# Performance work log

Measured on AMD Instinct MI355X. Metric: run time of the kernel, lower is better.

Reference implementation:

```python
import jax, jax.numpy as jnp
import numpy as np

N_NODES = 50000
N_EDGES = 600000
N_ELEMENTS = 100
N_RBF = 50
D = 128
CUTOFF = 5.0


def setup_inputs() -> dict:
    key = jax.random.key(0)
    ks = jax.random.split(key, 10)
    node_type = jax.random.randint(ks[0], (N_NODES,), 0, N_ELEMENTS)
    x_nodes = jax.random.normal(ks[1], (N_NODES, D), dtype=jnp.float32)
    src = jax.random.randint(ks[2], (N_EDGES,), 0, N_NODES)
    dst = jax.random.randint(ks[3], (N_EDGES,), 0, N_NODES)
    rbf_edges = jax.random.normal(ks[4], (N_EDGES, N_RBF), dtype=jnp.float32)
    dist = jax.random.uniform(ks[5], (N_EDGES,), dtype=jnp.float32) * (CUTOFF * 1.2)
    emb = jax.random.normal(ks[6], (N_ELEMENTS, D), dtype=jnp.float32) * 0.1
    W_e = jax.random.normal(ks[7], (D, N_RBF), dtype=jnp.float32) * (1.0 / np.sqrt(N_RBF))
    b_e = jnp.zeros((D,), dtype=jnp.float32)
    W_c = jax.random.normal(ks[8], (D, 2 * D), dtype=jnp.float32) * (1.0 / np.sqrt(2 * D))
    b_c = jnp.zeros((D,), dtype=jnp.float32)
    return {"node_type": node_type, "x_nodes": x_nodes, "src": src, "dst": dst,
            "rbf_edges": rbf_edges, "dist": dist, "emb": emb,
            "W_e": W_e, "b_e": b_e, "W_c": W_c, "b_c": b_c}


def cosine_cutoff(dist, cutoff):
    # 0.5*(cos(pi*d/cutoff)+1), zeroed beyond cutoff
    w = 0.5 * (jnp.cos(dist * (jnp.pi / cutoff)) + 1.0)
    return w * (dist < cutoff).astype(dist.dtype)


def reference(node_type, x_nodes, src, dst, rbf_edges, dist, emb, W_e, b_e, W_c, b_c):
    # node embedding from atom type: [N, D]
    x_neighbors = emb[node_type]
    # edge projection weighted by cutoff: [E, D]
    x_edges = (rbf_edges @ W_e.T + b_e) * cosine_cutoff(dist, CUTOFF)[:, None]
    # gather source node embedding, multiply by edge embedding, scatter-sum to dst
    msg = x_neighbors[src] * x_edges  # [E, D]
    x_integrated = jax.ops.segment_sum(msg, dst, num_segments=N_NODES)  # [N, D]
    # concat + combine linear: [N, D]
    x_combine = jnp.concatenate([x_nodes, x_integrated], axis=-1)
    return x_combine @ W_c.T + b_c
```

## Files before the change

kernel.cpp:

```cpp
#include <hip/hip_runtime.h>
#include <hip/hip_bf16.h>

constexpr int NN   = 50000;
constexpr int NE   = 600000;
constexpr int NRBF = 50;
constexpr int DIM  = 128;
constexpr float CUT = 5.0f;
constexpr float PI_F = 3.14159265358979323846f;

constexpr int CAP = 64;

constexpr size_t OFF_DEG  = 0;
constexpr size_t OFF_OVFC = OFF_DEG  + (size_t)NN * 4;
constexpr size_t OFF_EID  = 200960;
constexpr size_t OFF_OVF  = OFF_EID  + (size_t)NN * CAP * 4;
constexpr size_t OFF_MSG  = OFF_OVF  + (size_t)NE * 4;
constexpr size_t OFF_XI   = OFF_MSG  + (size_t)NE * DIM * 2;


typedef __attribute__((ext_vector_type(4))) float f32x4;
typedef __attribute__((ext_vector_type(8))) short short8;

__device__ __forceinline__ float bf2f(unsigned short u) {
    return __uint_as_float(((unsigned int)u) << 16);
}
__device__ __forceinline__ unsigned short f2bf(float f) {
    return __bfloat16_as_ushort(__float2bfloat16(f));
}

__global__ __launch_bounds__(256)
void build_buckets(const int* __restrict__ dst, const float* __restrict__ dist,
                   int* __restrict__ deg, int* __restrict__ eid,
                   int* __restrict__ ovf, int* __restrict__ ovf_cnt)
{
    const int e = blockIdx.x * 256 + threadIdx.x;
    if (e >= NE) return;
    if (dist[e] < CUT) {
        const int n = dst[e];
        const int pos = atomicAdd(&deg[n], 1);
        if (pos < CAP) eid[n * CAP + pos] = e;
        else           ovf[atomicAdd(ovf_cnt, 1)] = e;
    }
}

__global__ __launch_bounds__(256)
void edge_msg_kernel(const float* __restrict__ rbf, const float* __restrict__ dist,
                     const int* __restrict__ src, const int* __restrict__ node_type,
                     const float* __restrict__ emb, const float* __restrict__ W_e,
                     const float* __restrict__ b_e, __hip_bfloat16* __restrict__ msg)
{
    __shared__ unsigned short As[64][72];
    __shared__ unsigned short Bs[128][72];
    __shared__ float cc_s[64];
    __shared__ int   embrow_s[64];

    const int t  = threadIdx.x;
    const int wv = t >> 6, l = t & 63;
    const int col = l & 15;
    const int rq  = (l >> 4) * 4;

    {
        const int r = t >> 1, c = t & 1;
        const float2* row = (const float2*)(W_e + (size_t)r * NRBF);
        #pragma unroll
        for (int s = 0; s < 13; ++s) {
            const int idx = c + 2 * s;
            if (idx < 25) {
                const float2 v = row[idx];
                *(ushort2*)&Bs[r][2 * idx] = make_ushort2(f2bf(v.x), f2bf(v.y));
            }
        }
        #pragma unroll
        for (int q = 0; q < 4; ++q)
            *(ushort2*)&Bs[r][50 + 4 * q + 2 * c] = make_ushort2(0, 0);
    }

    float be[8];
    #pragma unroll
    for (int nt = 0; nt < 8; ++nt) be[nt] = b_e[nt * 16 + col];

    for (int tile = 0; tile < 4; ++tile) {
        const int e0 = (blockIdx.x * 4 + tile) * 64;
        if (e0 >= NE) break;
        if (tile) __syncthreads();

        {
            const int r = t >> 2, c = t & 3;
            const float2* row = (const float2*)(rbf + (size_t)(e0 + r) * NRBF);
            #pragma unroll
            for (int s = 0; s < 7; ++s) {
                const int idx = c + 4 * s;
                if (idx < 25) {
                    const float2 v = row[idx];
                    *(ushort2*)&As[r][2 * idx] = make_ushort2(f2bf(v.x), f2bf(v.y));
                }
            }
            *(ushort2*)&As[r][50 + 2 * c] = make_ushort2(0, 0);
            *(ushort2*)&As[r][58 + 2 * c] = make_ushort2(0, 0);
        }
        if (t < 64) {
            const int e = e0 + t;
            const float dd = dist[e];
            const float w  = 0.5f * (__cosf(dd * (PI_F / CUT)) + 1.0f);
            cc_s[t]     = (dd < CUT) ? w : 0.0f;
            embrow_s[t] = node_type[src[e]];
        }
        __syncthreads();

        f32x4 acc[8] = {};
        #pragma unroll
        for (int s = 0; s < 2; ++s) {
            const int ko = s * 32 + (l >> 4) * 8;
            const short8 af = *(const short8*)&As[wv * 16 + (l & 15)][ko];
            #pragma unroll
            for (int nt = 0; nt < 8; ++nt) {
                const short8 bf = *(const short8*)&Bs[nt * 16 + (l & 15)][ko];
                acc[nt] = __builtin_amdgcn_mfma_f32_16x16x32_bf16(af, bf, acc[nt], 0, 0, 0);
            }
        }

        #pragma unroll
        for (int r = 0; r < 4; ++r) {
            const int el = wv * 16 + rq + r;
            const float cc = cc_s[el];
            if (cc != 0.0f) {
                const int erow = embrow_s[el];
                unsigned int w[4];
                #pragma unroll
                for (int q = 0; q < 4; ++q) {
                    const float v0 = (acc[2 * q][r]     + be[2 * q])     * cc *
                                     emb[(size_t)erow * DIM + (2 * q) * 16 + col];
                    const float v1 = (acc[2 * q + 1][r] + be[2 * q + 1]) * cc *
                                     emb[(size_t)erow * DIM + (2 * q + 1) * 16 + col];
                    w[q] = (unsigned int)f2bf(v0) | ((unsigned int)f2bf(v1) << 16);
                }
                int4* dp = (int4*)(msg + (size_t)(e0 + el) * DIM + 8 * col);
                *dp = make_int4((int)w[0], (int)w[1], (int)w[2], (int)w[3]);
            }
        }
    }
}

__global__ __launch_bounds__(256)
void gather_sum(const __hip_bfloat16* __restrict__ msg, const int* __restrict__ deg,
                const int* __restrict__ eid, const int* __restrict__ ovf,
                const int* __restrict__ ovf_cnt, const int* __restrict__ dst,
                __hip_bfloat16* __restrict__ xi)
{
    const int t    = threadIdx.x;
    const int lane = t & 63;
    const int n    = blockIdx.x * 4 + (t >> 6);
    if (n >= NN) return;

    const int dn   = deg[n];
    const int degn = dn < CAP ? dn : CAP;
    int eidv = 0;
    if (lane < degn) eidv = eid[n * CAP + lane];

    float ax = 0.0f, ay = 0.0f;
    int j = 0;
    for (; j + 4 <= degn; j += 4) {
        const int ea = __shfl(eidv, j);
        const int eb = __shfl(eidv, j + 1);
        const int ec = __shfl(eidv, j + 2);
        const int ed = __shfl(eidv, j + 3);
        const ushort2 va = ((const ushort2*)(msg + (size_t)ea * DIM))[lane];
        const ushort2 vb = ((const ushort2*)(msg + (size_t)eb * DIM))[lane];
        const ushort2 vc = ((const ushort2*)(msg + (size_t)ec * DIM))[lane];
        const ushort2 vd = ((const ushort2*)(msg + (size_t)ed * DIM))[lane];
        ax += bf2f(va.x) + bf2f(vb.x) + bf2f(vc.x) + bf2f(vd.x);
        ay += bf2f(va.y) + bf2f(vb.y) + bf2f(vc.y) + bf2f(vd.y);
    }
    for (; j < degn; ++j) {
        const int e = __shfl(eidv, j);
        const ushort2 v = ((const ushort2*)(msg + (size_t)e * DIM))[lane];
        ax += bf2f(v.x);
        ay += bf2f(v.y);
    }
    const int ocnt = ovf_cnt[0];
    for (j = 0; j < ocnt; ++j) {
        const int e = ovf[j];
        if (dst[e] == n) {
            const ushort2 v = ((const ushort2*)(msg + (size_t)e * DIM))[lane];
            ax += bf2f(v.x);
            ay += bf2f(v.y);
        }
    }

    const int d0  = 2 * lane;
    const int p_a = ((d0 & 15) << 3) + (d0 >> 4);
    const int s0  = p_a >> 1;
    const int cmp = p_a & 1;
    const float A1 = __shfl(ax, s0);
    const float B1 = __shfl(ay, s0);
    const float A2 = __shfl(ax, s0 + 4);
    const float B2 = __shfl(ay, s0 + 4);
    const float va = cmp ? B1 : A1;
    const float vb = cmp ? B2 : A2;

    ((ushort2*)(xi + (size_t)n * DIM))[lane] = make_ushort2(f2bf(va), f2bf(vb));
}

__global__ __launch_bounds__(256)
void combine_mfma(const float* __restrict__ x_nodes, const __hip_bfloat16* __restrict__ xi,
                  const float* __restrict__ W_c, const float* __restrict__ b_c,
                  float* __restrict__ out)
{
    __shared__ unsigned short As[64][72];
    __shared__ unsigned short Bs[128][72];

    const int t  = threadIdx.x;
    const int wv = t >> 6;
    const int l  = t & 63;
    const int n0 = blockIdx.x * 64;

    f32x4 acc[8] = {};

    for (int kc = 0; kc < 4; ++kc) {
        const int kb = kc * 64;
        if (kc) __syncthreads();
        {
            const int r  = t >> 2;
            const int c0 = (t & 3) * 16;
            const int n  = n0 + r;
            if (kc < 2) {
                float4 v[4];
                if (n < NN) {
                    const float4* p = (const float4*)(x_nodes + (size_t)n * DIM + kb + c0);
                    v[0] = p[0]; v[1] = p[1]; v[2] = p[2]; v[3] = p[3];
                } else {
                    v[0] = v[1] = v[2] = v[3] = make_float4(0.f, 0.f, 0.f, 0.f);
                }
                unsigned short* dp = &As[r][c0];
                #pragma unroll
                for (int q = 0; q < 4; ++q) {
                    *(ushort2*)&dp[q * 4]     = make_ushort2(f2bf(v[q].x), f2bf(v[q].y));
                    *(ushort2*)&dp[q * 4 + 2] = make_ushort2(f2bf(v[q].z), f2bf(v[q].w));
                }
            } else {
                int4 v0 = make_int4(0, 0, 0, 0), v1 = make_int4(0, 0, 0, 0);
                if (n < NN) {
                    const int4* p = (const int4*)(xi + (size_t)n * DIM + (kb - DIM) + c0);
                    v0 = p[0];
                    v1 = p[1];
                }
                *(int4*)&As[r][c0]     = v0;
                *(int4*)&As[r][c0 + 8] = v1;
            }
        }
        {
            const int dch = t >> 1;
            const int c0  = (t & 1) * 32;
            const float4* p = (const float4*)(W_c + (size_t)dch * (2 * DIM) + kb + c0);
            unsigned short* dp = &Bs[dch][c0];
            #pragma unroll
            for (int q = 0; q < 8; ++q) {
                const float4 v = p[q];
                *(ushort2*)&dp[q * 4]     = make_ushort2(f2bf(v.x), f2bf(v.y));
                *(ushort2*)&dp[q * 4 + 2] = make_ushort2(f2bf(v.z), f2bf(v.w));
            }
        }
        __syncthreads();
        #pragma unroll
        for (int s = 0; s < 2; ++s) {
            const int ko = s * 32 + (l >> 4) * 8;
            const short8 af = *(const short8*)&As[wv * 16 + (l & 15)][ko];
            #pragma unroll
            for (int nt = 0; nt < 8; ++nt) {
                const short8 bf = *(const short8*)&Bs[nt * 16 + (l & 15)][ko];
                acc[nt] = __builtin_amdgcn_mfma_f32_16x16x32_bf16(af, bf, acc[nt], 0, 0, 0);
            }
        }
    }

    const int col = l & 15;
    const int rq  = (l >> 4) * 4;
    #pragma unroll
    for (int nt = 0; nt < 8; ++nt) {
        const int dim = nt * 16 + col;
        const float bc = b_c[dim];
        #pragma unroll
        for (int r = 0; r < 4; ++r) {
            const int node = n0 + wv * 16 + rq + r;
            if (node < NN)
                out[(size_t)node * DIM + dim] = acc[nt][r] + bc;
        }
    }
}

extern "C" void kernel_launch(void* const* d_in, const int* in_sizes, int n_in,
                              void* d_out, int out_size, void* d_ws, size_t ws_size,
                              hipStream_t stream)
{
    const int*   node_type = (const int*)  d_in[0];
    const float* x_nodes   = (const float*)d_in[1];
    const int*   src       = (const int*)  d_in[2];
    const int*   dst       = (const int*)  d_in[3];
    const float* rbf       = (const float*)d_in[4];
    const float* dist      = (const float*)d_in[5];
    const float* emb       = (const float*)d_in[6];
    const float* W_e       = (const float*)d_in[7];
    const float* b_e       = (const float*)d_in[8];
    const float* W_c       = (const float*)d_in[9];
    const float* b_c       = (const float*)d_in[10];
    float* out = (float*)d_out;

    char* ws = (char*)d_ws;
    int*            deg     = (int*)(ws + OFF_DEG);
    int*            ovf_cnt = (int*)(ws + OFF_OVFC);
    int*            eid     = (int*)(ws + OFF_EID);
    int*            ovf     = (int*)(ws + OFF_OVF);
    __hip_bfloat16* msg     = (__hip_bfloat16*)(ws + OFF_MSG);
    __hip_bfloat16* xi      = (__hip_bfloat16*)(ws + OFF_XI);

    hipMemsetAsync(deg, 0, (NN + 1) * sizeof(int), stream);

    build_buckets<<<(NE + 255) / 256, 256, 0, stream>>>(dst, dist, deg, eid, ovf, ovf_cnt);

    edge_msg_kernel<<<(NE / 64 + 3) / 4, 256, 0, stream>>>(rbf, dist, src, node_type, emb,
                                                           W_e, b_e, msg);

    gather_sum<<<(NN + 3) / 4, 256, 0, stream>>>(msg, deg, eid, ovf, ovf_cnt, dst, xi);

    combine_mfma<<<(NN + 63) / 64, 256, 0, stream>>>(x_nodes, xi, W_c, b_c, out);
}
```

Before: 357.6 us.

## Hold edge weights in registers, fold bias and cutoff into GEMM, vectorize gather

Adds a prep kernel that converts W_e into a bf16 matrix with the bias folded in as an extra K column, and builds a bf16 permuted embedding table. Cutoff weights and source embedding rows are now computed in build_buckets. The edge message kernel loads B fragments straight into registers and builds A fragments from rbf pre-scaled by the cutoff, removing shared memory and syncs. The gather kernel reads 16-byte vectors from four edges at a time and reduces them with cross-lane shuffles, and CAP drops to 32. This adds a launch and extra workspace traffic, and the smaller CAP could push more edges onto the slow overflow path.

```diff
diff --git a/kernel.cpp b/kernel.cpp
--- a/kernel.cpp
+++ b/kernel.cpp
@@ -8,14 +8,18 @@
 constexpr float CUT = 5.0f;
 constexpr float PI_F = 3.14159265358979323846f;
 
-constexpr int CAP = 64;
-
-constexpr size_t OFF_DEG  = 0;
-constexpr size_t OFF_OVFC = OFF_DEG  + (size_t)NN * 4;
-constexpr size_t OFF_EID  = 200960;
-constexpr size_t OFF_OVF  = OFF_EID  + (size_t)NN * CAP * 4;
-constexpr size_t OFF_MSG  = OFF_OVF  + (size_t)NE * 4;
-constexpr size_t OFF_XI   = OFF_MSG  + (size_t)NE * DIM * 2;
+constexpr int CAP = 32;
+
+constexpr size_t OFF_DEG   = 0;
+constexpr size_t OFF_OVFC  = (size_t)NN * 4;
+constexpr size_t OFF_EID   = 200960;
+constexpr size_t OFF_OVF   = OFF_EID  + (size_t)NN * CAP * 4;
+constexpr size_t OFF_CC    = OFF_OVF  + (size_t)NE * 4;
+constexpr size_t OFF_EROW  = OFF_CC   + (size_t)NE * 4;
+constexpr size_t OFF_WAUG  = OFF_EROW + (size_t)NE * 4;
+constexpr size_t OFF_EPERM = OFF_WAUG + 128 * 64 * 2;
+constexpr size_t OFF_MSG   = 13843200;
+constexpr size_t OFF_XI    = OFF_MSG  + (size_t)NE * DIM * 2;
 
 
 typedef __attribute__((ext_vector_type(4))) float f32x4;
@@ -29,13 +33,40 @@
 }
 
 __global__ __launch_bounds__(256)
+void prep_w(const float* __restrict__ W_e, const float* __restrict__ b_e,
+            const float* __restrict__ emb,
+            unsigned short* __restrict__ W_aug, unsigned short* __restrict__ emb_perm)
+{
+    const int tid = blockIdx.x * 256 + threadIdx.x;
+    if (tid < 128 * 64) {
+        const int d = tid >> 6, k = tid & 63;
+        float v = 0.0f;
+        if (k < NRBF)       v = W_e[d * NRBF + k];
+        else if (k == NRBF) v = b_e[d];
+        W_aug[tid] = f2bf(v);
+    } else if (tid < 128 * 64 + 100 * 128) {
+        const int i = tid - 128 * 64;
+        const int tau = i >> 7, p = i & 127;
+        const int d = 16 * (p & 7) + (p >> 3);
+        emb_perm[i] = f2bf(emb[tau * DIM + d]);
+    }
+}
+
+__global__ __launch_bounds__(256)
 void build_buckets(const int* __restrict__ dst, const float* __restrict__ dist,
+                   const int* __restrict__ src, const int* __restrict__ node_type,
                    int* __restrict__ deg, int* __restrict__ eid,
-                   int* __restrict__ ovf, int* __restrict__ ovf_cnt)
+                   int* __restrict__ ovf, int* __restrict__ ovf_cnt,
+                   float* __restrict__ cc_arr, int* __restrict__ embrow)
 {
     const int e = blockIdx.x * 256 + threadIdx.x;
     if (e >= NE) return;
-    if (dist[e] < CUT) {
+    const float dd = dist[e];
+    const bool act = dd < CUT;
+    const float w = 0.5f * (__cosf(dd * (PI_F / CUT)) + 1.0f);
+    cc_arr[e] = act ? w : 0.0f;
+    embrow[e] = act ? node_type[src[e]] : -1;
+    if (act) {
         const int n = dst[e];
         const int pos = atomicAdd(&deg[n], 1);
         if (pos < CAP) eid[n * CAP + pos] = e;
@@ -44,161 +75,155 @@
 }
 
 __global__ __launch_bounds__(256)
-void edge_msg_kernel(const float* __restrict__ rbf, const float* __restrict__ dist,
-                     const int* __restrict__ src, const int* __restrict__ node_type,
-                     const float* __restrict__ emb, const float* __restrict__ W_e,
-                     const float* __restrict__ b_e, __hip_bfloat16* __restrict__ msg)
-{
-    __shared__ unsigned short As[64][72];
-    __shared__ unsigned short Bs[128][72];
-    __shared__ float cc_s[64];
-    __shared__ int   embrow_s[64];
-
+void edge_msg_reg(const float* __restrict__ rbf,
+                  const float* __restrict__ cc_arr,
+                  const int* __restrict__ embrow,
+                  const unsigned short* __restrict__ W_aug,
+                  const unsigned short* __restrict__ emb_perm,
+                  unsigned short* __restrict__ msg)
+{
     const int t  = threadIdx.x;
     const int wv = t >> 6, l = t & 63;
-    const int col = l & 15;
-    const int rq  = (l >> 4) * 4;
-
-    {
-        const int r = t >> 1, c = t & 1;
-        const float2* row = (const float2*)(W_e + (size_t)r * NRBF);
+    const int c  = l & 15, g = l >> 4;
+
+    short8 bfrag[16];
+    #pragma unroll
+    for (int nt = 0; nt < 8; ++nt)
         #pragma unroll
-        for (int s = 0; s < 13; ++s) {
-            const int idx = c + 2 * s;
-            if (idx < 25) {
-                const float2 v = row[idx];
-                *(ushort2*)&Bs[r][2 * idx] = make_ushort2(f2bf(v.x), f2bf(v.y));
-            }
-        }
-        #pragma unroll
-        for (int q = 0; q < 4; ++q)
-            *(ushort2*)&Bs[r][50 + 4 * q + 2 * c] = make_ushort2(0, 0);
-    }
-
-    float be[8];
+        for (int s = 0; s < 2; ++s)
+            bfrag[nt * 2 + s] =
+                *(const short8*)(W_aug + (nt * 16 + c) * 64 + s * 32 + g * 8);
+
     #pragma unroll
-    for (int nt = 0; nt < 8; ++nt) be[nt] = b_e[nt * 16 + col];
-
     for (int tile = 0; tile < 4; ++tile) {
         const int e0 = (blockIdx.x * 4 + tile) * 64;
-        if (e0 >= NE) break;
-        if (tile) __syncthreads();
-
-        {
-            const int r = t >> 2, c = t & 3;
-            const float2* row = (const float2*)(rbf + (size_t)(e0 + r) * NRBF);
-            #pragma unroll
-            for (int s = 0; s < 7; ++s) {
-                const int idx = c + 4 * s;
-                if (idx < 25) {
-                    const float2 v = row[idx];
-                    *(ushort2*)&As[r][2 * idx] = make_ushort2(f2bf(v.x), f2bf(v.y));
+        if (e0 < NE) {
+            const int er = e0 + wv * 16 + c;
+            const float ccl = cc_arr[er];
+            const float* rp = rbf + (size_t)er * NRBF;
+
+            int erow[4];
+            #pragma unroll
+            for (int r = 0; r < 4; ++r)
+                erow[r] = embrow[e0 + wv * 16 + 4 * g + r];
+
+            const float2 r0 = *(const float2*)(rp + 8 * g);
+            const float2 r1 = *(const float2*)(rp + 8 * g + 2);
+            const float2 r2 = *(const float2*)(rp + 8 * g + 4);
+            const float2 r3 = *(const float2*)(rp + 8 * g + 6);
+            float2 q0 = make_float2(0.f, 0.f), q1 = q0, q2 = q0, q3 = q0;
+            if (g < 2) {
+                q0 = *(const float2*)(rp + 32 + 8 * g);
+                q1 = *(const float2*)(rp + 32 + 8 * g + 2);
+                q2 = *(const float2*)(rp + 32 + 8 * g + 4);
+                q3 = *(const float2*)(rp + 32 + 8 * g + 6);
+            } else if (g == 2) {
+                q0 = *(const float2*)(rp + 48);
+            }
+
+            short8 a0, a1;
+            a0[0] = (short)f2bf(ccl * r0.x); a0[1] = (short)f2bf(ccl * r0.y);
+            a0[2] = (short)f2bf(ccl * r1.x); a0[3] = (short)f2bf(ccl * r1.y);
+            a0[4] = (short)f2bf(ccl * r2.x); a0[5] = (short)f2bf(ccl * r2.y);
+            a0[6] = (short)f2bf(ccl * r3.x); a0[7] = (short)f2bf(ccl * r3.y);
+            a1[0] = (short)f2bf(ccl * q0.x); a1[1] = (short)f2bf(ccl * q0.y);
+            a1[2] = (short)f2bf(ccl * q1.x); a1[3] = (short)f2bf(ccl * q1.y);
+            a1[4] = (short)f2bf(ccl * q2.x); a1[5] = (short)f2bf(ccl * q2.y);
+            a1[6] = (short)f2bf(ccl * q3.x); a1[7] = (short)f2bf(ccl * q3.y);
+            if (g == 2) {
+                a1[2] = (short)f2bf(ccl);
+                a1[3] = 0; a1[4] = 0; a1[5] = 0; a1[6] = 0; a1[7] = 0;
+            }
+
+            f32x4 acc[8] = {};
+            #pragma unroll
+            for (int nt = 0; nt < 8; ++nt)
+                acc[nt] = __builtin_amdgcn_mfma_f32_16x16x32_bf16(a0, bfrag[nt * 2],
+                                                                  acc[nt], 0, 0, 0);
+            #pragma unroll
+            for (int nt = 0; nt < 8; ++nt)
+                acc[nt] = __builtin_amdgcn_mfma_f32_16x16x32_bf16(a1, bfrag[nt * 2 + 1],
+                                                                  acc[nt], 0, 0, 0);
+
+            #pragma unroll
+            for (int r = 0; r < 4; ++r) {
+                const int e = e0 + wv * 16 + 4 * g + r;
+                const int rw = erow[r];
+                if (rw >= 0) {
+                    const int4 em = *(const int4*)(emb_perm + rw * DIM + 8 * c);
+                    const unsigned int* ep = (const unsigned int*)&em;
+                    unsigned int ow[4];
+                    #pragma unroll
+                    for (int q = 0; q < 4; ++q) {
+                        const float m0 = bf2f((unsigned short)(ep[q] & 0xffff));
+                        const float m1 = bf2f((unsigned short)(ep[q] >> 16));
+                        const float v0 = acc[2 * q][r] * m0;
+                        const float v1 = acc[2 * q + 1][r] * m1;
+                        ow[q] = (unsigned int)f2bf(v0) | ((unsigned int)f2bf(v1) << 16);
+                    }
+                    *(int4*)(msg + (size_t)e * DIM + 8 * c) =
+                        make_int4((int)ow[0], (int)ow[1], (int)ow[2], (int)ow[3]);
                 }
             }
-            *(ushort2*)&As[r][50 + 2 * c] = make_ushort2(0, 0);
-            *(ushort2*)&As[r][58 + 2 * c] = make_ushort2(0, 0);
-        }
-        if (t < 64) {
-            const int e = e0 + t;
-            const float dd = dist[e];
-            const float w  = 0.5f * (__cosf(dd * (PI_F / CUT)) + 1.0f);
-            cc_s[t]     = (dd < CUT) ? w : 0.0f;
-            embrow_s[t] = node_type[src[e]];
-        }
-        __syncthreads();
-
-        f32x4 acc[8] = {};
-        #pragma unroll
-        for (int s = 0; s < 2; ++s) {
-            const int ko = s * 32 + (l >> 4) * 8;
-            const short8 af = *(const short8*)&As[wv * 16 + (l & 15)][ko];
-            #pragma unroll
-            for (int nt = 0; nt < 8; ++nt) {
-                const short8 bf = *(const short8*)&Bs[nt * 16 + (l & 15)][ko];
-                acc[nt] = __builtin_amdgcn_mfma_f32_16x16x32_bf16(af, bf, acc[nt], 0, 0, 0);
-            }
-        }
-
-        #pragma unroll
-        for (int r = 0; r < 4; ++r) {
-            const int el = wv * 16 + rq + r;
-            const float cc = cc_s[el];
-            if (cc != 0.0f) {
-                const int erow = embrow_s[el];
-                unsigned int w[4];
-                #pragma unroll
-                for (int q = 0; q < 4; ++q) {
-                    const float v0 = (acc[2 * q][r]     + be[2 * q])     * cc *
-                                     emb[(size_t)erow * DIM + (2 * q) * 16 + col];
-                    const float v1 = (acc[2 * q + 1][r] + be[2 * q + 1]) * cc *
-                                     emb[(size_t)erow * DIM + (2 * q + 1) * 16 + col];
-                    w[q] = (unsigned int)f2bf(v0) | ((unsigned int)f2bf(v1) << 16);
-                }
-                int4* dp = (int4*)(msg + (size_t)(e0 + el) * DIM + 8 * col);
-                *dp = make_int4((int)w[0], (int)w[1], (int)w[2], (int)w[3]);
-            }
-        }
-    }
-}
-
-__global__ __launch_bounds__(256)
-void gather_sum(const __hip_bfloat16* __restrict__ msg, const int* __restrict__ deg,
+        }
+    }
+}
+
+__global__ __launch_bounds__(256)
+void gather_sum(const unsigned short* __restrict__ msg, const int* __restrict__ deg,
                 const int* __restrict__ eid, const int* __restrict__ ovf,
                 const int* __restrict__ ovf_cnt, const int* __restrict__ dst,
-                __hip_bfloat16* __restrict__ xi)
-{
-    const int t    = threadIdx.x;
-    const int lane = t & 63;
-    const int n    = blockIdx.x * 4 + (t >> 6);
+                unsigned short* __restrict__ xi)
+{
+    const int t = threadIdx.x, l = t & 63;
+    const int c = l & 15, g = l >> 4;
+    const int n = blockIdx.x * 4 + (t >> 6);
     if (n >= NN) return;
 
     const int dn   = deg[n];
     const int degn = dn < CAP ? dn : CAP;
     int eidv = 0;
-    if (lane < degn) eidv = eid[n * CAP + lane];
-
-    float ax = 0.0f, ay = 0.0f;
-    int j = 0;
-    for (; j + 4 <= degn; j += 4) {
-        const int ea = __shfl(eidv, j);
-        const int eb = __shfl(eidv, j + 1);
-        const int ec = __shfl(eidv, j + 2);
-        const int ed = __shfl(eidv, j + 3);
-        const ushort2 va = ((const ushort2*)(msg + (size_t)ea * DIM))[lane];
-        const ushort2 vb = ((const ushort2*)(msg + (size_t)eb * DIM))[lane];
-        const ushort2 vc = ((const ushort2*)(msg + (size_t)ec * DIM))[lane];
-        const ushort2 vd = ((const ushort2*)(msg + (size_t)ed * DIM))[lane];
-        ax += bf2f(va.x) + bf2f(vb.x) + bf2f(vc.x) + bf2f(vd.x);
-        ay += bf2f(va.y) + bf2f(vb.y) + bf2f(vc.y) + bf2f(vd.y);
-    }
-    for (; j < degn; ++j) {
-        const int e = __shfl(eidv, j);
-        const ushort2 v = ((const ushort2*)(msg + (size_t)e * DIM))[lane];
-        ax += bf2f(v.x);
-        ay += bf2f(v.y);
+    if (l < degn) eidv = eid[n * CAP + l];
+
+    float v[8] = {};
+    for (int j = 0; j < degn; j += 4) {
+        const int e = __shfl(eidv, j + g);
+        if (j + g < degn) {
+            const int4 mv = *(const int4*)(msg + (size_t)e * DIM + 8 * c);
+            const unsigned int* mp = (const unsigned int*)&mv;
+            #pragma unroll
+            for (int q = 0; q < 4; ++q) {
+                v[2 * q]     += bf2f((unsigned short)(mp[q] & 0xffff));
+                v[2 * q + 1] += bf2f((unsigned short)(mp[q] >> 16));
+            }
+        }
     }
     const int ocnt = ovf_cnt[0];
-    for (j = 0; j < ocnt; ++j) {
+    for (int j = 0; j < ocnt; ++j) {
         const int e = ovf[j];
-        if (dst[e] == n) {
-            const ushort2 v = ((const ushort2*)(msg + (size_t)e * DIM))[lane];
-            ax += bf2f(v.x);
-            ay += bf2f(v.y);
-        }
-    }
-
-    const int d0  = 2 * lane;
-    const int p_a = ((d0 & 15) << 3) + (d0 >> 4);
-    const int s0  = p_a >> 1;
-    const int cmp = p_a & 1;
-    const float A1 = __shfl(ax, s0);
-    const float B1 = __shfl(ay, s0);
-    const float A2 = __shfl(ax, s0 + 4);
-    const float B2 = __shfl(ay, s0 + 4);
-    const float va = cmp ? B1 : A1;
-    const float vb = cmp ? B2 : A2;
-
-    ((ushort2*)(xi + (size_t)n * DIM))[lane] = make_ushort2(f2bf(va), f2bf(vb));
+        if (g == 0 && dst[e] == n) {
+            const int4 mv = *(const int4*)(msg + (size_t)e * DIM + 8 * c);
+            const unsigned int* mp = (const unsigned int*)&mv;
+            #pragma unroll
+            for (int q = 0; q < 4; ++q) {
+                v[2 * q]     += bf2f((unsigned short)(mp[q] & 0xffff));
+                v[2 * q + 1] += bf2f((unsigned short)(mp[q] >> 16));
+            }
+        }
+    }
+
+    #pragma unroll
+    for (int q = 0; q < 8; ++q) {
+        v[q] += __shfl_xor(v[q], 16);
+        v[q] += __shfl_xor(v[q], 32);
+    }
+
+    float s0 = v[0], s1 = v[1];
+    if (g == 1)      { s0 = v[2]; s1 = v[3]; }
+    else if (g == 2) { s0 = v[4]; s1 = v[5]; }
+    else if (g == 3) { s0 = v[6]; s1 = v[7]; }
+    xi[(size_t)n * DIM + 32 * g + c]      = f2bf(s0);
+    xi[(size_t)n * DIM + 32 * g + 16 + c] = f2bf(s1);
 }
 
 __global__ __launch_bounds__(256)
@@ -306,21 +331,29 @@
     float* out = (float*)d_out;
 
     char* ws = (char*)d_ws;
-    int*            deg     = (int*)(ws + OFF_DEG);
-    int*            ovf_cnt = (int*)(ws + OFF_OVFC);
-    int*            eid     = (int*)(ws + OFF_EID);
-    int*            ovf     = (int*)(ws + OFF_OVF);
-    __hip_bfloat16* msg     = (__hip_bfloat16*)(ws + OFF_MSG);
-    __hip_bfloat16* xi      = (__hip_bfloat16*)(ws + OFF_XI);
+    int*            deg      = (int*)(ws + OFF_DEG);
+    int*            ovf_cnt  = (int*)(ws + OFF_OVFC);
+    int*            eid      = (int*)(ws + OFF_EID);
+    int*            ovf      = (int*)(ws + OFF_OVF);
+    float*          cc_arr   = (float*)(ws + OFF_CC);
+    int*            embrow   = (int*)(ws + OFF_EROW);
+    unsigned short* W_aug    = (unsigned short*)(ws + OFF_WAUG);
+    unsigned short* emb_perm = (unsigned short*)(ws + OFF_EPERM);
+    unsigned short* msg      = (unsigned short*)(ws + OFF_MSG);
+    unsigned short* xi       = (unsigned short*)(ws + OFF_XI);
 
     hipMemsetAsync(deg, 0, (NN + 1) * sizeof(int), stream);
 
-    build_buckets<<<(NE + 255) / 256, 256, 0, stream>>>(dst, dist, deg, eid, ovf, ovf_cnt);
-
-    edge_msg_kernel<<<(NE / 64 + 3) / 4, 256, 0, stream>>>(rbf, dist, src, node_type, emb,
-                                                           W_e, b_e, msg);
+    prep_w<<<82, 256, 0, stream>>>(W_e, b_e, emb, W_aug, emb_perm);
+
+    build_buckets<<<(NE + 255) / 256, 256, 0, stream>>>(
+        dst, dist, src, node_type, deg, eid, ovf, ovf_cnt, cc_arr, embrow);
+
+    edge_msg_reg<<<(NE / 64 + 3) / 4, 256, 0, stream>>>(
+        rbf, cc_arr, embrow, W_aug, emb_perm, msg);
 
     gather_sum<<<(NN + 3) / 4, 256, 0, stream>>>(msg, deg, eid, ovf, ovf_cnt, dst, xi);
 
-    combine_mfma<<<(NN + 63) / 64, 256, 0, stream>>>(x_nodes, xi, W_c, b_c, out);
-}
+    combine_mfma<<<(NN + 63) / 64, 256, 0, stream>>>(
+        x_nodes, (const __hip_bfloat16*)xi, W_c, b_c, out);
+}
```

Result: no change. 355.3 us (-0.6%).
